# Optimization experiments

Hardware: AMD Instinct MI355X
Metric: run time of the kernel (lower is better)

Reference implementation:

```python
import jax, jax.numpy as jnp
import numpy as np

WS = 8          # window size
N = WS * WS     # tokens per window (64)
C = 256         # embed dim
H = 8           # heads
D = C // H      # head dim (32)
NW = 256        # windows per image
B_ = 2048       # total windows in batch (8 images * 256 windows)
CPB_HIDDEN = 512


def _make_relative_position_index():
    coords_h = np.arange(WS)
    coords_w = np.arange(WS)
    coords = np.stack(np.meshgrid(coords_h, coords_w, indexing='ij'))  # [2,WS,WS]
    coords = coords.reshape(2, -1)                                     # [2,N]
    rel = coords[:, :, None] - coords[:, None, :]                      # [2,N,N]
    rel = rel.transpose(1, 2, 0).astype(np.int64)                      # [N,N,2]
    rel[:, :, 0] += WS - 1
    rel[:, :, 1] += WS - 1
    rel[:, :, 0] *= 2 * WS - 1
    return rel.sum(-1)                                                 # [N,N]


def _make_relative_coords_table():
    rh = np.arange(-(WS - 1), WS, dtype=np.float64)
    rw = np.arange(-(WS - 1), WS, dtype=np.float64)
    tbl = np.stack(np.meshgrid(rh, rw, indexing='ij')).transpose(1, 2, 0)[None]  # [1,2W-1,2W-1,2]
    tbl[:, :, :, 0] /= (WS - 1)  # pretrained_window_size == window_size
    tbl[:, :, :, 1] /= (WS - 1)
    tbl *= 8
    tbl = np.sign(tbl) * np.log2(np.abs(tbl) + 1.0) / np.log2(8)
    return tbl.astype(np.float32)


def setup_inputs() -> dict:
    key = jax.random.key(0)
    ks = jax.random.split(key, 8)
    x = jax.random.normal(ks[0], (B_, N, C), dtype=jnp.float32)
    # shifted-window style additive mask: 0 for allowed, -100 for masked
    mask_bits = jax.random.uniform(ks[1], (NW, N, N)) < 0.1
    mask = jnp.where(mask_bits, jnp.float32(-100.0), jnp.float32(0.0))
    qkv_w = jax.random.normal(ks[2], (C, 3 * C), dtype=jnp.float32) * (1.0 / np.sqrt(C))
    q_bias = jnp.zeros((C,), jnp.float32)
    v_bias = jnp.zeros((C,), jnp.float32)
    logit_scale = jnp.full((H, 1, 1), np.log(10.0), dtype=jnp.float32)
    coords_table = jnp.asarray(_make_relative_coords_table())
    mlp1_w = jax.random.normal(ks[3], (2, CPB_HIDDEN), dtype=jnp.float32) * 0.5
    mlp1_b = jnp.zeros((CPB_HIDDEN,), jnp.float32)
    mlp2_w = jax.random.normal(ks[4], (CPB_HIDDEN, H), dtype=jnp.float32) * (1.0 / np.sqrt(CPB_HIDDEN))
    proj_w = jax.random.normal(ks[5], (C, C), dtype=jnp.float32) * (1.0 / np.sqrt(C))
    proj_b = jnp.zeros((C,), jnp.float32)
    rel_pos_index = jnp.asarray(_make_relative_position_index())  # [N,N] int64
    return {
        'x': x, 'mask': mask, 'qkv_w': qkv_w, 'q_bias': q_bias, 'v_bias': v_bias,
        'logit_scale': logit_scale, 'coords_table': coords_table,
        'mlp1_w': mlp1_w, 'mlp1_b': mlp1_b, 'mlp2_w': mlp2_w,
        'proj_w': proj_w, 'proj_b': proj_b, 'rel_pos_index': rel_pos_index,
    }


def _l2norm(t, axis=-1, eps=1e-12):
    n = jnp.sqrt(jnp.sum(t * t, axis=axis, keepdims=True))
    return t / jnp.maximum(n, eps)


def reference(x, mask, qkv_w, q_bias, v_bias, logit_scale, coords_table,
              mlp1_w, mlp1_b, mlp2_w, proj_w, proj_b, rel_pos_index):
    b, n, c = x.shape
    # qkv projection with (q_bias, 0, v_bias)
    qkv_bias = jnp.concatenate([q_bias, jnp.zeros_like(v_bias), v_bias], axis=0)
    qkv = x @ qkv_w + qkv_bias                          # [b, n, 3c]
    qkv = qkv.reshape(b, n, 3, H, D).transpose(2, 0, 3, 1, 4)  # [3, b, H, n, D]
    q, k, v = qkv[0], qkv[1], qkv[2]
    # cosine attention with learned per-head logit scale
    attn = jnp.einsum('bhnd,bhmd->bhnm', _l2norm(q), _l2norm(k))
    scale = jnp.exp(jnp.minimum(logit_scale, jnp.float32(np.log(1.0 / 0.01))))  # [H,1,1]
    attn = attn * scale[None]                           # [b, H, n, n]
    # continuous position bias MLP
    hbt = jax.nn.relu(coords_table @ mlp1_w + mlp1_b)   # [1, 2W-1, 2W-1, 512]
    bias_table = (hbt @ mlp2_w).reshape(-1, H)          # [(2W-1)^2, H]
    rel_bias = bias_table[rel_pos_index.reshape(-1)].reshape(n, n, H)
    rel_bias = 16.0 * jax.nn.sigmoid(rel_bias.transpose(2, 0, 1))  # [H, n, n]
    attn = attn + rel_bias[None]
    # shifted-window mask
    nw = mask.shape[0]
    attn = attn.reshape(b // nw, nw, H, n, n) + mask[None, :, None]
    attn = attn.reshape(b, H, n, n)
    attn = jax.nn.softmax(attn, axis=-1)
    out = jnp.einsum('bhnm,bhmd->bnhd', attn, v).reshape(b, n, c)
    return out @ proj_w + proj_b
```

## Files before the change

kernel.cpp:

```cpp
#include <hip/hip_runtime.h>
#include <hip/hip_bf16.h>
#include <stdint.h>

#define NTOK   64
#define CDIM   256
#define NHEAD  8
#define DHEAD  32
#define NWIN   256
#define BWIN   2048
#define MROWS  131072

typedef __attribute__((ext_vector_type(8))) short short8;
typedef __attribute__((ext_vector_type(4))) float f32x4;

__device__ __forceinline__ ushort f2bf(float f) {
  uint32_t u = __float_as_uint(f);
  u += 0x7fffu + ((u >> 16) & 1u);
  return (ushort)(u >> 16);
}
__device__ __forceinline__ void unpack8(uint4 u, float* f) {
  f[0] = __uint_as_float(u.x << 16);
  f[1] = __uint_as_float(u.x & 0xffff0000u);
  f[2] = __uint_as_float(u.y << 16);
  f[3] = __uint_as_float(u.y & 0xffff0000u);
  f[4] = __uint_as_float(u.z << 16);
  f[5] = __uint_as_float(u.z & 0xffff0000u);
  f[6] = __uint_as_float(u.w << 16);
  f[7] = __uint_as_float(u.w & 0xffff0000u);
}


__global__ void k_cast_bf16(const float* __restrict__ src, ushort* __restrict__ dst, int n4) {
  int i = blockIdx.x * blockDim.x + threadIdx.x;
  int stride = gridDim.x * blockDim.x;
  for (; i < n4; i += stride) {
    float4 v = ((const float4*)src)[i];
    ushort4 o;
    o.x = f2bf(v.x); o.y = f2bf(v.y); o.z = f2bf(v.z); o.w = f2bf(v.w);
    ((ushort4*)dst)[i] = o;
  }
}

__global__ void k_transpose_bf16(const float* __restrict__ src, ushort* __restrict__ dst, int K, int N) {
  int idx = blockIdx.x * 256 + threadIdx.x;
  if (idx < N * K) {
    int n = idx / K, k = idx - n * K;
    dst[idx] = f2bf(src[(size_t)k * N + n]);
  }
}

__global__ void k_cpb(const float* __restrict__ ct, const float* __restrict__ w1,
                      const float* __restrict__ b1, const float* __restrict__ w2,
                      float* __restrict__ out) {
  int p = blockIdx.x, t = threadIdx.x;
  float c0 = ct[p * 2], c1 = ct[p * 2 + 1];
  float acc[8];
#pragma unroll
  for (int h = 0; h < 8; ++h) acc[h] = 0.f;
  for (int j = t; j < 512; j += 256) {
    float hj = fmaxf(0.f, fmaf(c0, w1[j], fmaf(c1, w1[512 + j], b1[j])));
#pragma unroll
    for (int h = 0; h < 8; ++h) acc[h] = fmaf(hj, w2[j * 8 + h], acc[h]);
  }
#pragma unroll
  for (int off = 1; off < 64; off <<= 1)
#pragma unroll
    for (int h = 0; h < 8; ++h) acc[h] += __shfl_xor(acc[h], off, 64);
  __shared__ float red[4][8];
  if ((t & 63) == 0)
#pragma unroll
    for (int h = 0; h < 8; ++h) red[t >> 6][h] = acc[h];
  __syncthreads();
  if (t < 8) out[p * 8 + t] = red[0][t] + red[1][t] + red[2][t] + red[3][t];
}

__global__ void k_relbC(const float* __restrict__ bt, const int* __restrict__ rpi,
                        float* __restrict__ out) {
  int idx = blockIdx.x * 256 + threadIdx.x;
  int reg = idx & 3, l16 = (idx >> 2) & 15, g = (idx >> 6) & 3;
  int nt = (idx >> 8) & 3, mt = (idx >> 10) & 3, h = idx >> 12;
  int r = mt * 16 + g * 4 + reg, c = nt * 16 + l16;
  float v = bt[rpi[r * 64 + c] * 8 + h];
  out[idx] = 16.0f / (1.0f + __expf(-v));
}

__global__ void k_maskC(const float* __restrict__ mask, float* __restrict__ out) {
  int idx = blockIdx.x * 256 + threadIdx.x;
  int reg = idx & 3, l16 = (idx >> 2) & 15, g = (idx >> 6) & 3;
  int nt = (idx >> 8) & 3, mt = (idx >> 10) & 3, wi = idx >> 12;
  int r = mt * 16 + g * 4 + reg, c = nt * 16 + l16;
  out[idx] = mask[(size_t)wi * 4096 + r * 64 + c];
}

template <int MODE>
__global__ __launch_bounds__(256, 2) void gemm_bt(const ushort* __restrict__ A,
                                                  const ushort* __restrict__ BT,
                                                  void* __restrict__ Cout,
                                                  const float* __restrict__ bias0,
                                                  const float* __restrict__ bias1,
                                                  int K, int N) {
  __shared__ ushort As[128 * 64];
  __shared__ ushort Bs[128 * 64];
  const int t = threadIdx.x;
  const int bn = blockIdx.x, bm = blockIdx.y;
  const int wv = t >> 6, lane = t & 63, quad = lane >> 4, l16 = lane & 15;
  const int mbase = (wv & 1) * 64, nbase = (wv >> 1) * 64;

  f32x4 acc[4][4] = {};

  const int nkt = K >> 6;
  for (int kt = 0; kt < nkt; ++kt) {
    __syncthreads();
#pragma unroll
    for (int i = 0; i < 4; ++i) {
      int idx = i * 256 + t;
      int m = idx >> 3, c = idx & 7;
      int sw = (m * 8 + (c ^ (m & 7))) * 8;
      *(uint4*)(As + sw) = *(const uint4*)(A + (size_t)(bm * 128 + m) * K + kt * 64 + c * 8);
      *(uint4*)(Bs + sw) = *(const uint4*)(BT + (size_t)(bn * 128 + m) * K + kt * 64 + c * 8);
    }
    __syncthreads();
#pragma unroll
    for (int k2 = 0; k2 < 2; ++k2) {
      const int cidx = (k2 * 4 + quad) ^ (l16 & 7);
      short8 a[4], b[4];
#pragma unroll
      for (int mt = 0; mt < 4; ++mt)
        a[mt] = *(const short8*)(As + ((mbase + mt * 16 + l16) * 8 + cidx) * 8);
#pragma unroll
      for (int nt = 0; nt < 4; ++nt)
        b[nt] = *(const short8*)(Bs + ((nbase + nt * 16 + l16) * 8 + cidx) * 8);
#pragma unroll
      for (int mt = 0; mt < 4; ++mt)
#pragma unroll
        for (int nt = 0; nt < 4; ++nt)
          acc[mt][nt] = __builtin_amdgcn_mfma_f32_16x16x32_bf16(a[mt], b[nt], acc[mt][nt], 0, 0, 0);
    }
  }

#pragma unroll
  for (int mt = 0; mt < 4; ++mt)
#pragma unroll
    for (int nt = 0; nt < 4; ++nt) {
      int j = bn * 128 + nbase + nt * 16 + l16;
      int gm = bm * 128 + mbase + mt * 16 + quad * 4;
      float bs;
      if (MODE == 0) bs = (j < 256) ? bias0[j] : ((j < 512) ? 0.0f : bias1[j - 512]);
      else bs = bias0[j];
#pragma unroll
      for (int i2 = 0; i2 < 4; ++i2) {
        float v = acc[mt][nt][i2] + bs;
        size_t off = (size_t)(gm + i2) * N + j;
        if (MODE == 0) ((ushort*)Cout)[off] = f2bf(v);
        else ((float*)Cout)[off] = v;
      }
    }
}

__global__ __launch_bounds__(256, 2) void k_attn_mfma(const ushort* __restrict__ qkv,
                                                      const float* __restrict__ maskC,
                                                      const float* __restrict__ ls,
                                                      const float* __restrict__ relbC,
                                                      ushort* __restrict__ aob) {
  __shared__ ushort Qs[4][64][40];
  __shared__ ushort Ks[4][64][40];
  __shared__ ushort Vt[4][32][72];
  __shared__ ushort Ps[4][64][40];
  const int b = blockIdx.x, t = threadIdx.x;
  const int wi = b & (NWIN - 1);
  const int wv = t >> 6, lane = t & 63;
  const int g = lane >> 4, l16 = lane & 15;

  for (int pass = 0; pass < 2; ++pass) {
    __syncthreads();
    {
      const int hh = wv, tok = lane;
      const int h = pass * 4 + hh;
      const size_t base = ((size_t)b * 64 + tok) * 768 + h * 32;
      {
        union { uint4 u[4]; ushort s[32]; } raw, outp;
        raw.u[0] = *(const uint4*)(qkv + base);
        raw.u[1] = *(const uint4*)(qkv + base + 8);
        raw.u[2] = *(const uint4*)(qkv + base + 16);
        raw.u[3] = *(const uint4*)(qkv + base + 24);
        float f[32];
#pragma unroll
        for (int c = 0; c < 4; ++c) unpack8(raw.u[c], f + c * 8);
        float s = 0.f;
#pragma unroll
        for (int j = 0; j < 32; ++j) s = fmaf(f[j], f[j], s);
        float sc = __expf(fminf(ls[h], 4.6051701859880914f));
        float fac = sc / fmaxf(sqrtf(s), 1e-12f);
#pragma unroll
        for (int j = 0; j < 32; ++j) outp.s[j] = f2bf(f[j] * fac);
#pragma unroll
        for (int c = 0; c < 4; ++c) *(uint4*)&Qs[hh][tok][c * 8] = outp.u[c];
      }
      {
        union { uint4 u[4]; ushort s[32]; } raw, outp;
        raw.u[0] = *(const uint4*)(qkv + base + 256);
        raw.u[1] = *(const uint4*)(qkv + base + 264);
        raw.u[2] = *(const uint4*)(qkv + base + 272);
        raw.u[3] = *(const uint4*)(qkv + base + 280);
        float f[32];
#pragma unroll
        for (int c = 0; c < 4; ++c) unpack8(raw.u[c], f + c * 8);
        float s = 0.f;
#pragma unroll
        for (int j = 0; j < 32; ++j) s = fmaf(f[j], f[j], s);
        float fac = 1.0f / fmaxf(sqrtf(s), 1e-12f);
#pragma unroll
        for (int j = 0; j < 32; ++j) outp.s[j] = f2bf(f[j] * fac);
#pragma unroll
        for (int c = 0; c < 4; ++c) *(uint4*)&Ks[hh][tok][c * 8] = outp.u[c];
      }
      {
        union { uint4 u[4]; ushort s[32]; } raw;
        raw.u[0] = *(const uint4*)(qkv + base + 512);
        raw.u[1] = *(const uint4*)(qkv + base + 520);
        raw.u[2] = *(const uint4*)(qkv + base + 528);
        raw.u[3] = *(const uint4*)(qkv + base + 536);
#pragma unroll
        for (int d = 0; d < 32; ++d) Vt[hh][d][tok] = raw.s[d];
      }
    }
    __syncthreads();

    const int h = pass * 4 + wv;
    short8 qfr[4], kfr[4];
#pragma unroll
    for (int mt = 0; mt < 4; ++mt) qfr[mt] = *(const short8*)&Qs[wv][mt * 16 + l16][g * 8];
#pragma unroll
    for (int nt = 0; nt < 4; ++nt) kfr[nt] = *(const short8*)&Ks[wv][nt * 16 + l16][g * 8];
    f32x4 sv[4][4];
    const f32x4 zero = {0.f, 0.f, 0.f, 0.f};
#pragma unroll
    for (int mt = 0; mt < 4; ++mt)
#pragma unroll
      for (int nt = 0; nt < 4; ++nt)
        sv[mt][nt] = __builtin_amdgcn_mfma_f32_16x16x32_bf16(qfr[mt], kfr[nt], zero, 0, 0, 0);

#pragma unroll
    for (int mt = 0; mt < 4; ++mt)
#pragma unroll
      for (int nt = 0; nt < 4; ++nt) {
        float4 rb = *(const float4*)(relbC + (size_t)(((h * 4 + mt) * 4 + nt) * 4 + g) * 64 + l16 * 4);
        float4 mk = *(const float4*)(maskC + (size_t)(((wi * 4 + mt) * 4 + nt) * 4 + g) * 64 + l16 * 4);
        sv[mt][nt][0] += rb.x + mk.x;
        sv[mt][nt][1] += rb.y + mk.y;
        sv[mt][nt][2] += rb.z + mk.z;
        sv[mt][nt][3] += rb.w + mk.w;
      }

    float mx[4][4], inv[4][4];
#pragma unroll
    for (int mt = 0; mt < 4; ++mt)
#pragma unroll
      for (int reg = 0; reg < 4; ++reg) {
        float m = fmaxf(fmaxf(sv[mt][0][reg], sv[mt][1][reg]),
                        fmaxf(sv[mt][2][reg], sv[mt][3][reg]));
#pragma unroll
        for (int st = 1; st < 16; st <<= 1) m = fmaxf(m, __shfl_xor(m, st, 64));
        mx[mt][reg] = m;
      }
#pragma unroll
    for (int mt = 0; mt < 4; ++mt)
#pragma unroll
      for (int nt = 0; nt < 4; ++nt)
#pragma unroll
        for (int reg = 0; reg < 4; ++reg)
          sv[mt][nt][reg] = __expf(sv[mt][nt][reg] - mx[mt][reg]);
#pragma unroll
    for (int mt = 0; mt < 4; ++mt)
#pragma unroll
      for (int reg = 0; reg < 4; ++reg) {
        float s = sv[mt][0][reg] + sv[mt][1][reg] + sv[mt][2][reg] + sv[mt][3][reg];
#pragma unroll
        for (int st = 1; st < 16; st <<= 1) s += __shfl_xor(s, st, 64);
        inv[mt][reg] = 1.0f / s;
      }

    f32x4 ov[4][2] = {};
#pragma unroll
    for (int kt = 0; kt < 2; ++kt) {
      __syncthreads();
#pragma unroll
      for (int mt = 0; mt < 4; ++mt)
#pragma unroll
        for (int reg = 0; reg < 4; ++reg)
#pragma unroll
          for (int tjh = 0; tjh < 2; ++tjh)
            Ps[wv][mt * 16 + g * 4 + reg][tjh * 16 + l16] = f2bf(sv[mt][kt * 2 + tjh][reg]);
      __syncthreads();
      short8 pf[4], vf[2];
#pragma unroll
      for (int mt = 0; mt < 4; ++mt) pf[mt] = *(const short8*)&Ps[wv][mt * 16 + l16][g * 8];
#pragma unroll
      for (int n2 = 0; n2 < 2; ++n2) vf[n2] = *(const short8*)&Vt[wv][n2 * 16 + l16][kt * 32 + g * 8];
#pragma unroll
      for (int mt = 0; mt < 4; ++mt)
#pragma unroll
        for (int n2 = 0; n2 < 2; ++n2)
          ov[mt][n2] = __builtin_amdgcn_mfma_f32_16x16x32_bf16(pf[mt], vf[n2], ov[mt][n2], 0, 0, 0);
    }

#pragma unroll
    for (int mt = 0; mt < 4; ++mt)
#pragma unroll
      for (int n2 = 0; n2 < 2; ++n2)
#pragma unroll
        for (int reg = 0; reg < 4; ++reg) {
          int r = mt * 16 + g * 4 + reg;
          float o = ov[mt][n2][reg] * inv[mt][reg];
          aob[((size_t)b * 64 + r) * 256 + h * 32 + n2 * 16 + l16] = f2bf(o);
        }
  }
}


extern "C" void kernel_launch(void* const* d_in, const int* in_sizes, int n_in,
                              void* d_out, int out_size, void* d_ws, size_t ws_size,
                              hipStream_t stream) {
  const float* x      = (const float*)d_in[0];
  const float* mask   = (const float*)d_in[1];
  const float* qkv_w  = (const float*)d_in[2];
  const float* q_bias = (const float*)d_in[3];
  const float* v_bias = (const float*)d_in[4];
  const float* lscale = (const float*)d_in[5];
  const float* ctbl   = (const float*)d_in[6];
  const float* m1w    = (const float*)d_in[7];
  const float* m1b    = (const float*)d_in[8];
  const float* m2w    = (const float*)d_in[9];
  const float* projw  = (const float*)d_in[10];
  const float* projb  = (const float*)d_in[11];
  const int*   rpi    = (const int*)d_in[12];

  char* w = (char*)d_ws;
  float*  bias_table = (float*)(w + 0);
  float*  relbC      = (float*)(w + 8192);
  float*  maskC      = (float*)(w + 139264);
  ushort* qkvWT      = (ushort*)(w + 4333568);
  ushort* projWT     = (ushort*)(w + 4726784);
  ushort* xb         = (ushort*)(w + 4857856);
  ushort* qkvb       = (ushort*)(w + 71966720ull);
  ushort* aob        = (ushort*)(w + 273293312ull);
  (void)ws_size; (void)n_in; (void)in_sizes; (void)out_size;

  k_cast_bf16<<<4096, 256, 0, stream>>>(x, xb, MROWS * CDIM / 4);
  k_transpose_bf16<<<768, 256, 0, stream>>>(qkv_w, qkvWT, 256, 768);
  k_transpose_bf16<<<256, 256, 0, stream>>>(projw, projWT, 256, 256);
  k_cpb<<<225, 256, 0, stream>>>(ctbl, m1w, m1b, m2w, bias_table);
  k_relbC<<<128, 256, 0, stream>>>(bias_table, rpi, relbC);
  k_maskC<<<4096, 256, 0, stream>>>(mask, maskC);

  gemm_bt<0><<<dim3(6, 1024), 256, 0, stream>>>(xb, qkvWT, qkvb, q_bias, v_bias, 256, 768);
  k_attn_mfma<<<BWIN, 256, 0, stream>>>(qkvb, maskC, lscale, relbC, aob);
  gemm_bt<1><<<dim3(2, 1024), 256, 0, stream>>>(aob, projWT, d_out, projb, nullptr, 256, 256);
}
```

Before: 504.4 us.

## Load Q/K fragments directly into registers, use direct-to-LDS GEMM loads, swizzle workgroups

The GEMM now loads A/B tiles through global_load_lds (direct global-to-LDS) with the XOR swizzle moved to the global address, and remaps workgroup IDs across groups of 8 to improve cache locality. The attention kernel drops the Q/K shared buffers: each lane loads its MFMA fragment straight from global memory and computes the L2 norm with cross-lane shuffles. It also removes block-wide barriers, since each wave only touches its own LDS slice, and raises the occupancy hint to 4 blocks. The risk is that removing the barriers relies on wave-private LDS regions, which holds here because each wave indexes only its own slice.

```diff
diff --git a/kernel.cpp b/kernel.cpp
--- a/kernel.cpp
+++ b/kernel.cpp
@@ -27,6 +27,12 @@
   f[5] = __uint_as_float(u.z & 0xffff0000u);
   f[6] = __uint_as_float(u.w << 16);
   f[7] = __uint_as_float(u.w & 0xffff0000u);
+}
+
+__device__ __forceinline__ void gload_lds16(const ushort* g, ushort* l) {
+  __builtin_amdgcn_global_load_lds(
+      (const __attribute__((address_space(1))) void*)g,
+      (__attribute__((address_space(3))) void*)l, 16, 0, 0);
 }
 
 
@@ -102,7 +108,13 @@
   __shared__ ushort As[128 * 64];
   __shared__ ushort Bs[128 * 64];
   const int t = threadIdx.x;
-  const int bn = blockIdx.x, bm = blockIdx.y;
+
+  const int gx = gridDim.x;
+  int wg = blockIdx.y * gx + blockIdx.x;
+  const int nwg = gx * gridDim.y;
+  if ((nwg & 7) == 0) wg = (wg & 7) * (nwg >> 3) + (wg >> 3);
+  const int bm = wg / gx, bn = wg - bm * gx;
+
   const int wv = t >> 6, lane = t & 63, quad = lane >> 4, l16 = lane & 15;
   const int mbase = (wv & 1) * 64, nbase = (wv >> 1) * 64;
 
@@ -115,9 +127,10 @@
     for (int i = 0; i < 4; ++i) {
       int idx = i * 256 + t;
       int m = idx >> 3, c = idx & 7;
-      int sw = (m * 8 + (c ^ (m & 7))) * 8;
-      *(uint4*)(As + sw) = *(const uint4*)(A + (size_t)(bm * 128 + m) * K + kt * 64 + c * 8);
-      *(uint4*)(Bs + sw) = *(const uint4*)(BT + (size_t)(bn * 128 + m) * K + kt * 64 + c * 8);
+      int cg = c ^ (m & 7);
+      int ldsoff = (i * 256 + (t & ~63)) * 8;
+      gload_lds16(A + (size_t)(bm * 128 + m) * K + kt * 64 + cg * 8, As + ldsoff);
+      gload_lds16(BT + (size_t)(bn * 128 + m) * K + kt * 64 + cg * 8, Bs + ldsoff);
     }
     __syncthreads();
 #pragma unroll
@@ -157,81 +170,69 @@
     }
 }
 
-__global__ __launch_bounds__(256, 2) void k_attn_mfma(const ushort* __restrict__ qkv,
+__global__ __launch_bounds__(256, 4) void k_attn_mfma(const ushort* __restrict__ qkv,
                                                       const float* __restrict__ maskC,
                                                       const float* __restrict__ ls,
                                                       const float* __restrict__ relbC,
                                                       ushort* __restrict__ aob) {
-  __shared__ ushort Qs[4][64][40];
-  __shared__ ushort Ks[4][64][40];
   __shared__ ushort Vt[4][32][72];
   __shared__ ushort Ps[4][64][40];
   const int b = blockIdx.x, t = threadIdx.x;
   const int wi = b & (NWIN - 1);
   const int wv = t >> 6, lane = t & 63;
   const int g = lane >> 4, l16 = lane & 15;
+  const size_t rowb = (size_t)b * 64;
 
   for (int pass = 0; pass < 2; ++pass) {
-    __syncthreads();
+    const int h = pass * 4 + wv;
+
     {
-      const int hh = wv, tok = lane;
-      const int h = pass * 4 + hh;
-      const size_t base = ((size_t)b * 64 + tok) * 768 + h * 32;
-      {
-        union { uint4 u[4]; ushort s[32]; } raw, outp;
-        raw.u[0] = *(const uint4*)(qkv + base);
-        raw.u[1] = *(const uint4*)(qkv + base + 8);
-        raw.u[2] = *(const uint4*)(qkv + base + 16);
-        raw.u[3] = *(const uint4*)(qkv + base + 24);
-        float f[32];
-#pragma unroll
-        for (int c = 0; c < 4; ++c) unpack8(raw.u[c], f + c * 8);
-        float s = 0.f;
-#pragma unroll
-        for (int j = 0; j < 32; ++j) s = fmaf(f[j], f[j], s);
-        float sc = __expf(fminf(ls[h], 4.6051701859880914f));
-        float fac = sc / fmaxf(sqrtf(s), 1e-12f);
-#pragma unroll
-        for (int j = 0; j < 32; ++j) outp.s[j] = f2bf(f[j] * fac);
-#pragma unroll
-        for (int c = 0; c < 4; ++c) *(uint4*)&Qs[hh][tok][c * 8] = outp.u[c];
-      }
-      {
-        union { uint4 u[4]; ushort s[32]; } raw, outp;
-        raw.u[0] = *(const uint4*)(qkv + base + 256);
-        raw.u[1] = *(const uint4*)(qkv + base + 264);
-        raw.u[2] = *(const uint4*)(qkv + base + 272);
-        raw.u[3] = *(const uint4*)(qkv + base + 280);
-        float f[32];
-#pragma unroll
-        for (int c = 0; c < 4; ++c) unpack8(raw.u[c], f + c * 8);
-        float s = 0.f;
-#pragma unroll
-        for (int j = 0; j < 32; ++j) s = fmaf(f[j], f[j], s);
-        float fac = 1.0f / fmaxf(sqrtf(s), 1e-12f);
-#pragma unroll
-        for (int j = 0; j < 32; ++j) outp.s[j] = f2bf(f[j] * fac);
-#pragma unroll
-        for (int c = 0; c < 4; ++c) *(uint4*)&Ks[hh][tok][c * 8] = outp.u[c];
-      }
-      {
-        union { uint4 u[4]; ushort s[32]; } raw;
-        raw.u[0] = *(const uint4*)(qkv + base + 512);
-        raw.u[1] = *(const uint4*)(qkv + base + 520);
-        raw.u[2] = *(const uint4*)(qkv + base + 528);
-        raw.u[3] = *(const uint4*)(qkv + base + 536);
-#pragma unroll
-        for (int d = 0; d < 32; ++d) Vt[hh][d][tok] = raw.s[d];
-      }
-    }
-    __syncthreads();
-
-    const int h = pass * 4 + wv;
+      const int tok = lane;
+      const size_t base = (rowb + tok) * 768 + 512 + h * 32;
+      union { uint4 u[4]; ushort s[32]; } raw;
+      raw.u[0] = *(const uint4*)(qkv + base);
+      raw.u[1] = *(const uint4*)(qkv + base + 8);
+      raw.u[2] = *(const uint4*)(qkv + base + 16);
+      raw.u[3] = *(const uint4*)(qkv + base + 24);
+#pragma unroll
+      for (int d = 0; d < 32; ++d) Vt[wv][d][tok] = raw.s[d];
+    }
+
+    const float sc = __expf(fminf(ls[h], 4.6051701859880914f));
     short8 qfr[4], kfr[4];
 #pragma unroll
-    for (int mt = 0; mt < 4; ++mt) qfr[mt] = *(const short8*)&Qs[wv][mt * 16 + l16][g * 8];
-#pragma unroll
-    for (int nt = 0; nt < 4; ++nt) kfr[nt] = *(const short8*)&Ks[wv][nt * 16 + l16][g * 8];
+    for (int mt = 0; mt < 4; ++mt) {
+      uint4 r = *(const uint4*)(qkv + (rowb + mt * 16 + l16) * 768 + h * 32 + g * 8);
+      float f[8];
+      unpack8(r, f);
+      float s = 0.f;
+#pragma unroll
+      for (int j = 0; j < 8; ++j) s = fmaf(f[j], f[j], s);
+      s += __shfl_xor(s, 16, 64);
+      s += __shfl_xor(s, 32, 64);
+      const float fac = sc / fmaxf(sqrtf(s), 1e-12f);
+      union { short8 v; ushort us[8]; } o;
+#pragma unroll
+      for (int j = 0; j < 8; ++j) o.us[j] = f2bf(f[j] * fac);
+      qfr[mt] = o.v;
+    }
+#pragma unroll
+    for (int nt = 0; nt < 4; ++nt) {
+      uint4 r = *(const uint4*)(qkv + (rowb + nt * 16 + l16) * 768 + 256 + h * 32 + g * 8);
+      float f[8];
+      unpack8(r, f);
+      float s = 0.f;
+#pragma unroll
+      for (int j = 0; j < 8; ++j) s = fmaf(f[j], f[j], s);
+      s += __shfl_xor(s, 16, 64);
+      s += __shfl_xor(s, 32, 64);
+      const float fac = 1.0f / fmaxf(sqrtf(s), 1e-12f);
+      union { short8 v; ushort us[8]; } o;
+#pragma unroll
+      for (int j = 0; j < 8; ++j) o.us[j] = f2bf(f[j] * fac);
+      kfr[nt] = o.v;
+    }
+
     f32x4 sv[4][4];
     const f32x4 zero = {0.f, 0.f, 0.f, 0.f};
 #pragma unroll
@@ -283,7 +284,6 @@
     f32x4 ov[4][2] = {};
 #pragma unroll
     for (int kt = 0; kt < 2; ++kt) {
-      __syncthreads();
 #pragma unroll
       for (int mt = 0; mt < 4; ++mt)
 #pragma unroll
@@ -291,7 +291,6 @@
 #pragma unroll
           for (int tjh = 0; tjh < 2; ++tjh)
             Ps[wv][mt * 16 + g * 4 + reg][tjh * 16 + l16] = f2bf(sv[mt][kt * 2 + tjh][reg]);
-      __syncthreads();
       short8 pf[4], vf[2];
 #pragma unroll
       for (int mt = 0; mt < 4; ++mt) pf[mt] = *(const short8*)&Ps[wv][mt * 16 + l16][g * 8];
```

Result: slower. 609.7 us (+20.9%).
